# Optimization experiments

Hardware: AMD Instinct MI355X
Metric: run time of the kernel (lower is better)

## Reference

```python
import jax, jax.numpy as jnp
import numpy as np


def _dwconv(x, w, b):
    # depthwise conv, NCHW, kernel [C,1,k,k], SAME padding k//2
    k = w.shape[-1]
    p = k // 2
    out = jax.lax.conv_general_dilated(x, w, (1, 1), [(p, p), (p, p)],
                                       feature_group_count=x.shape[1])
    return out + b[None, :, None, None]


def _conv1x1(x, W, b):
    return jnp.einsum('oc,bchw->bohw', W, x) + b[None, :, None, None]


def _ca_weight(q, k):
    # q,k: [b,c,h,w] -> energy [b,h,w,h+w]
    eH = jnp.einsum('bchw,bcgw->bhwg', q, k)  # attend along H (column)
    eW = jnp.einsum('bchw,bchv->bhwv', q, k)  # attend along W (row)
    return jnp.concatenate([eH, eW], axis=3)


def _ca_map(att, v):
    # att: [b,h,w,h+w], v: [b,c,h,w]
    h = v.shape[2]
    outH = jnp.einsum('bcgw,bhwg->bchw', v, att[..., :h])
    outW = jnp.einsum('bchv,bhwv->bchw', v, att[..., h:])
    return outH + outW


def _cc_block(cnn, Wq, bq, Wk, bk, Wv, bv, gamma):
    q = _conv1x1(cnn, Wq, bq)
    k = _conv1x1(cnn, Wk, bk)
    v = _conv1x1(cnn, Wv, bv)
    att = jax.nn.softmax(_ca_weight(q, k), axis=1)  # softmax over H axis, as in torch F.softmax(energy, 1)
    return gamma * _ca_map(att, v) + cnn


def _ppeg(x, w7, b7, w5, b5, w3, b3, H, W):
    C = x.shape[1]
    cnn = x.T.reshape(1, C, H, W)
    out = _dwconv(cnn, w7, b7) + cnn + _dwconv(cnn, w5, b5) + _dwconv(cnn, w3, b3)
    return out.reshape(C, H * W).T  # [N, C]


def setup_inputs() -> dict:
    key = jax.random.key(0)
    N, DIM, HID, QK = 65536, 1024, 512, 64  # N = 256^2
    ks = jax.random.split(key, 26)
    s = 0.02
    inp = {
        'h0': jax.random.normal(ks[0], (N, DIM), jnp.float32),
        'w7': jax.random.normal(ks[1], (DIM, 1, 7, 7)) * s,
        'b7': jax.random.normal(ks[2], (DIM,)) * s,
        'w5': jax.random.normal(ks[3], (DIM, 1, 5, 5)) * s,
        'b5': jax.random.normal(ks[4], (DIM,)) * s,
        'w3': jax.random.normal(ks[5], (DIM, 1, 3, 3)) * s,
        'b3': jax.random.normal(ks[6], (DIM,)) * s,
        'W1': jax.random.normal(ks[7], (HID, DIM)) * s,
        'b1': jax.random.normal(ks[8], (HID,)) * s,
        'Wq': jax.random.normal(ks[9], (QK, HID)) * s,
        'bq': jax.random.normal(ks[10], (QK,)) * s,
        'Wk': jax.random.normal(ks[11], (QK, HID)) * s,
        'bk': jax.random.normal(ks[12], (QK,)) * s,
        'Wv': jax.random.normal(ks[13], (HID, HID)) * s,
        'bv': jax.random.normal(ks[14], (HID,)) * s,
        'gamma': jax.random.normal(ks[15], ()) * 0.5,
        'Wq1': jax.random.normal(ks[16], (QK, HID)) * s,
        'bq1': jax.random.normal(ks[17], (QK,)) * s,
        'Wk1': jax.random.normal(ks[18], (QK, HID)) * s,
        'bk1': jax.random.normal(ks[19], (QK,)) * s,
        'Wv1': jax.random.normal(ks[20], (HID, HID)) * s,
        'bv1': jax.random.normal(ks[21], (HID,)) * s,
        'gamma1': jax.random.normal(ks[22], ()) * 0.5,
        'Wfc': jax.random.normal(ks[23], (1, HID)) * s,
        'bfc': jax.random.normal(ks[24], (1,)) * s,
    }
    return inp


def reference(h0, w7, b7, w5, b5, w3, b3, W1, b1,
              Wq, bq, Wk, bk, Wv, bv, gamma,
              Wq1, bq1, Wk1, bk1, Wv1, bv1, gamma1, Wfc, bfc):
    N = h0.shape[0]
    side = int(np.ceil(np.sqrt(N)))
    pad = side * side - N
    h1 = jnp.concatenate([h0, h0[:pad]], axis=0) if pad > 0 else h0
    # PPEG positional encoding (multi-kernel depthwise conv)
    h1 = _ppeg(h1, w7, b7, w5, b5, w3, b3, side, side)
    # fc1: Linear(1024->512) + ReLU  (h1 already square -> second pad is no-op)
    h2 = jax.nn.relu(h1 @ W1.T + b1)  # [N, 512]
    # CCAttention (two criss-cross blocks + fc to 1 logit)
    cnn = h2.T.reshape(1, h2.shape[1], side, side)
    out = _cc_block(cnn, Wq, bq, Wk, bk, Wv, bv, gamma)
    out1 = _cc_block(out, Wq1, bq1, Wk1, bk1, Wv1, bv1, gamma1)
    out1 = out1.reshape(out1.shape[1], side * side).T  # [N, 512]
    logits = out1 @ Wfc.T + bfc  # [N, 1]
    A = jax.nn.softmax(logits.T, axis=1)  # [1, N] attention over instances
    return A
```

## Files before the change

### kernel.cpp

```cpp
#include <hip/hip_runtime.h>

#define HW 65536
#define SIDE 256

typedef __attribute__((ext_vector_type(8))) short short8v;
typedef __attribute__((ext_vector_type(4))) float f32x4;
typedef __attribute__((ext_vector_type(8))) ushort ushort8v;

__device__ __forceinline__ ushort f2bf(float f) {
  unsigned int u = __builtin_bit_cast(unsigned int, f);
  u = (u + 0x7fff + ((u >> 16) & 1)) >> 16;
  return (ushort)u;
}
__device__ __forceinline__ float bf2f(unsigned int u) {
  return __builtin_bit_cast(float, (u & 0xffffu) << 16);
}
__device__ __forceinline__ float bflo(unsigned int d) {
  return __builtin_bit_cast(float, d << 16);
}
__device__ __forceinline__ float bfhi(unsigned int d) {
  return __builtin_bit_cast(float, d & 0xffff0000u);
}
__device__ __forceinline__ void gld16(const void* g, void* l) {
  __builtin_amdgcn_global_load_lds(
      (const __attribute__((address_space(1))) void*)g,
      (__attribute__((address_space(3))) void*)l, 16, 0, 0);
}

__global__ __launch_bounds__(256) void k_prep(
    const float* __restrict__ W1, const float* __restrict__ Wv,
    const float* __restrict__ Wv1, const float* __restrict__ Wq,
    const float* __restrict__ Wk, const float* __restrict__ Wq1,
    const float* __restrict__ Wk1, const float* __restrict__ bq,
    const float* __restrict__ bk, const float* __restrict__ bq1,
    const float* __restrict__ bk1, const float* __restrict__ w7,
    const float* __restrict__ b7, const float* __restrict__ w5,
    const float* __restrict__ b5, const float* __restrict__ w3,
    const float* __restrict__ b3,
    ushort* __restrict__ W1b, ushort* __restrict__ Wvb,
    ushort* __restrict__ Wv1b, ushort* __restrict__ Wqkb,
    ushort* __restrict__ Wqk1b, float* __restrict__ bqk,
    float* __restrict__ bqk1, float* __restrict__ wc, float* __restrict__ bc) {
  const int i = blockIdx.x * 256 + threadIdx.x;
  if (i < 524288) { W1b[i] = f2bf(W1[i]); return; }
  if (i < 786432) { int j = i - 524288; Wvb[j] = f2bf(Wv[j]); return; }
  if (i < 1048576) { int j = i - 786432; Wv1b[j] = f2bf(Wv1[j]); return; }
  if (i < 1081344) { int j = i - 1048576; Wqkb[j] = f2bf(Wq[j]); return; }
  if (i < 1114112) { int j = i - 1081344; Wqkb[32768 + j] = f2bf(Wk[j]); return; }
  if (i < 1146880) { int j = i - 1114112; Wqk1b[j] = f2bf(Wq1[j]); return; }
  if (i < 1179648) { int j = i - 1146880; Wqk1b[32768 + j] = f2bf(Wk1[j]); return; }
  if (i < 1179904) {
    int j = i - 1179648;
    if (j < 64) bqk[j] = bq[j];
    else if (j < 128) bqk[j] = bk[j - 64];
    else if (j < 192) bqk1[j - 128] = bq1[j - 128];
    else bqk1[j - 128] = bk1[j - 192];
    return;
  }
  if (i < 1180928) {
    const int c = i - 1179904;
    float w[49];
#pragma unroll
    for (int t = 0; t < 49; t++) w[t] = w7[c * 49 + t];
    for (int dy = 0; dy < 5; dy++)
      for (int dx = 0; dx < 5; dx++)
        w[(dy + 1) * 7 + (dx + 1)] += w5[c * 25 + dy * 5 + dx];
    for (int dy = 0; dy < 3; dy++)
      for (int dx = 0; dx < 3; dx++)
        w[(dy + 2) * 7 + (dx + 2)] += w3[c * 9 + dy * 3 + dx];
    w[3 * 7 + 3] += 1.0f;
#pragma unroll
    for (int t = 0; t < 49; t++) wc[c * 49 + t] = w[t];
    bc[c] = b7[c] + b5[c] + b3[c];
  }
}

__global__ __launch_bounds__(256) void k_transpose_nc_v(
    const float* __restrict__ in, ushort* __restrict__ out) {
  __shared__ ushort t[64][64];
  const int c0 = blockIdx.x << 6, r0 = blockIdx.y << 6;
  const int tid = threadIdx.x;
#pragma unroll
  for (int p = 0; p < 2; p++) {
    const int r = (tid >> 3) + p * 32, c8 = tid & 7;
    const float4 f0 = *(const float4*)&in[(size_t)(r0 + r) * 1024 + c0 + c8 * 8];
    const float4 f1 = *(const float4*)&in[(size_t)(r0 + r) * 1024 + c0 + c8 * 8 + 4];
    ushort8v v;
    v[0] = f2bf(f0.x); v[1] = f2bf(f0.y); v[2] = f2bf(f0.z); v[3] = f2bf(f0.w);
    v[4] = f2bf(f1.x); v[5] = f2bf(f1.y); v[6] = f2bf(f1.z); v[7] = f2bf(f1.w);
    *(ushort8v*)&t[r][(c8 ^ ((r >> 3) & 7)) * 8] = v;
  }
  __syncthreads();
#pragma unroll
  for (int p = 0; p < 2; p++) {
    const int c = (tid >> 3) + p * 32, r8 = tid & 7;
    ushort8v v;
#pragma unroll
    for (int j = 0; j < 8; j++) {
      const int rr = r8 * 8 + j;
      v[j] = t[rr][(((c >> 3) ^ r8) << 3) + (c & 7)];
    }
    *(ushort8v*)&out[(size_t)(c0 + c) * HW + r0 + r8 * 8] = v;
  }
}

__global__ __launch_bounds__(256) void k_trv(const ushort* __restrict__ in,
    ushort* __restrict__ out, int R, int C, long long bs) {
  __shared__ ushort t[64][64];
  const size_t base = (size_t)blockIdx.z * bs;
  const int c0 = blockIdx.x << 6, r0 = blockIdx.y << 6;
  const int tid = threadIdx.x;
#pragma unroll
  for (int p = 0; p < 2; p++) {
    const int r = (tid >> 3) + p * 32, c8 = tid & 7;
    const ushort8v v = *(const ushort8v*)&in[base + (size_t)(r0 + r) * C + c0 + c8 * 8];
    *(ushort8v*)&t[r][(c8 ^ ((r >> 3) & 7)) * 8] = v;
  }
  __syncthreads();
#pragma unroll
  for (int p = 0; p < 2; p++) {
    const int c = (tid >> 3) + p * 32, r8 = tid & 7;
    ushort8v v;
#pragma unroll
    for (int j = 0; j < 8; j++) {
      const int rr = r8 * 8 + j;
      v[j] = t[rr][(((c >> 3) ^ r8) << 3) + (c & 7)];
    }
    *(ushort8v*)&out[base + (size_t)(c0 + c) * R + r0 + r8 * 8] = v;
  }
}

__global__ __launch_bounds__(256) void k_dwconv7(const ushort* __restrict__ X,
    const float* __restrict__ wc, const float* __restrict__ bc,
    ushort* __restrict__ out) {
  __shared__ ushort tile[38][272];
  const int c = blockIdx.y;
  const int y0 = blockIdx.x << 5;
  const int tid = threadIdx.x;
  const ushort* Xc = X + (size_t)c * HW;

  float w[49];
#pragma unroll
  for (int i = 0; i < 49; i++) w[i] = wc[c * 49 + i];
  const float bcv = bc[c];

  if (tid < 76) {
    const int r = tid >> 1;
    ushort8v z = {0, 0, 0, 0, 0, 0, 0, 0};
    *(ushort8v*)&tile[r][(tid & 1) ? 264 : 0] = z;
  }
  for (int i = tid; i < 38 * 32; i += 256) {
    const int r = i >> 5, j8 = i & 31;
    const int y = y0 - 3 + r;
    ushort8v v = {0, 0, 0, 0, 0, 0, 0, 0};
    if (y >= 0 && y < SIDE) v = *(const ushort8v*)&Xc[y * SIDE + j8 * 8];
    *(ushort8v*)&tile[r][8 + j8 * 8] = v;
  }
  __syncthreads();

  const int t0 = tid & 63;
  const int ry = (tid >> 6) << 3;
  float acc[8][4] = {};
#pragma unroll
  for (int r = 0; r < 14; r++) {
    const uint2 ua = *(const uint2*)&tile[ry + r][(t0 << 2) + 4];
    const uint2 ub = *(const uint2*)&tile[ry + r][(t0 << 2) + 8];
    const uint2 uc = *(const uint2*)&tile[ry + r][(t0 << 2) + 12];
    float rv[12];
    rv[0] = bflo(ua.x); rv[1] = bfhi(ua.x); rv[2] = bflo(ua.y); rv[3] = bfhi(ua.y);
    rv[4] = bflo(ub.x); rv[5] = bfhi(ub.x); rv[6] = bflo(ub.y); rv[7] = bfhi(ub.y);
    rv[8] = bflo(uc.x); rv[9] = bfhi(uc.x); rv[10] = bflo(uc.y); rv[11] = bfhi(uc.y);
#pragma unroll
    for (int m = 0; m < 8; m++) {
      const int dy = r - m;
      if (dy < 0 || dy > 6) continue;
#pragma unroll
      for (int dx = 0; dx < 7; dx++) {
        const float ww = w[dy * 7 + dx];
#pragma unroll
        for (int o = 0; o < 4; o++) acc[m][o] += ww * rv[o + 1 + dx];
      }
    }
  }
#pragma unroll
  for (int m = 0; m < 8; m++) {
    ushort4 o4 = {f2bf(acc[m][0] + bcv), f2bf(acc[m][1] + bcv),
                  f2bf(acc[m][2] + bcv), f2bf(acc[m][3] + bcv)};
    *(ushort4*)&out[(size_t)c * HW + (y0 + ry + m) * SIDE + (t0 << 2)] = o4;
  }
}

template <int BN, int BIAS, int RELU, int OUTF, int OUTB, int SWZ, int TRN>
__global__ __launch_bounds__(256) void k_mm(
    const ushort* __restrict__ A, int lda, long long bsA,
    const ushort* __restrict__ B, int ldb, long long bsB,
    const float* __restrict__ bias,
    float* __restrict__ Cf, ushort* __restrict__ Cb, int ldc, long long bsC,
    ushort* __restrict__ Ct, int ldt, int K) {
  static_assert(BN == 64 || BN == 128, "BN");
  static_assert(!TRN || BN == 128, "TRN needs BN=128");
  constexpr int FN = BN / 32;
  __shared__ __align__(16) ushort SMEM[128 * 32 + BN * 32];
  ushort* As = SMEM;
  ushort* Bs = SMEM + 128 * 32;
  const int tid = threadIdx.x;

  int bx, by, bz;
  if constexpr (SWZ == 0) {
    bx = blockIdx.x; by = blockIdx.y; bz = blockIdx.z;
  } else if constexpr (SWZ == 1) {
    const int id = blockIdx.x, l = id >> 3;
    by = (id & 7) * 64 + (l >> 2); bx = l & 3; bz = 0;
  } else if constexpr (SWZ == 2) {
    const int id = blockIdx.x, l = id >> 3;
    bz = (id & 7) * 32 + (l >> 2); bx = l & 1; by = (l >> 1) & 1;
  } else {
    const int id = blockIdx.x, l = id >> 3;
    bz = (id & 7) * 32 + (l >> 3); bx = l & 3; by = (l >> 2) & 1;
  }

  const int bm = bx << 7, bn = by * BN;
  const long long zA = (long long)bz * bsA;
  const long long zB = (long long)bz * bsB;
  const long long zC = (long long)bz * bsC;

  const int sr = tid >> 2, sq = tid & 3;
  const int sw0 = (sr >> 1) & 3;
  const int sw1 = ((sr + 64) >> 1) & 3;
  const ushort* Ap0 = A + zA + (size_t)(bm + sr) * lda + ((sq ^ sw0) << 3);
  const ushort* Ap1 = A + zA + (size_t)(bm + sr + 64) * lda + ((sq ^ sw1) << 3);
  const ushort* Bp0 = B + zB + (size_t)(bn + sr) * ldb + ((sq ^ sw0) << 3);
  const ushort* Bp1 = nullptr;
  if constexpr (BN == 128)
    Bp1 = B + zB + (size_t)(bn + sr + 64) * ldb + ((sq ^ sw1) << 3);
  ushort* wA0 = &As[sr * 32 + sq * 8];
  ushort* wA1 = &As[(sr + 64) * 32 + sq * 8];
  ushort* wB0 = &Bs[sr * 32 + sq * 8];
  ushort* wB1 = nullptr;
  if constexpr (BN == 128) wB1 = &Bs[(sr + 64) * 32 + sq * 8];

  const int lane = tid & 63, wv = tid >> 6;
  const int wm = wv & 1, wn = wv >> 1;
  const int fr = lane & 15, kq = lane >> 4;
  int offA[4], offB[FN];
#pragma unroll
  for (int mi = 0; mi < 4; mi++) {
    const int row = wm * 64 + mi * 16 + fr;
    offA[mi] = row * 32 + ((kq ^ ((row >> 1) & 3)) << 3);
  }
#pragma unroll
  for (int ni = 0; ni < FN; ni++) {
    const int row = wn * (BN / 2) + ni * 16 + fr;
    offB[ni] = row * 32 + ((kq ^ ((row >> 1) & 3)) << 3);
  }

  f32x4 acc[4][FN];
#pragma unroll
  for (int mi = 0; mi < 4; mi++)
#pragma unroll
    for (int ni = 0; ni < FN; ni++) acc[mi][ni] = (f32x4){0.f, 0.f, 0.f, 0.f};

  for (int k0 = 0; k0 < K; k0 += 32) {
    __syncthreads();
    gld16(Ap0 + k0, wA0);
    gld16(Ap1 + k0, wA1);
    gld16(Bp0 + k0, wB0);
    if constexpr (BN == 128) gld16(Bp1 + k0, wB1);
    __syncthreads();
    short8v a[4], b[FN];
#pragma unroll
    for (int mi = 0; mi < 4; mi++) a[mi] = *(const short8v*)&As[offA[mi]];
#pragma unroll
    for (int ni = 0; ni < FN; ni++) b[ni] = *(const short8v*)&Bs[offB[ni]];
#pragma unroll
    for (int mi = 0; mi < 4; mi++)
#pragma unroll
      for (int ni = 0; ni < FN; ni++)
        acc[mi][ni] = __builtin_amdgcn_mfma_f32_16x16x32_bf16(b[ni], a[mi], acc[mi][ni], 0, 0, 0);
  }

  ushort tb[4][FN][4];
#pragma unroll
  for (int mi = 0; mi < 4; mi++) {
    const int row = bm + wm * 64 + mi * 16 + fr;
    const float bs1 = (BIAS == 1) ? bias[row] : 0.f;
#pragma unroll
    for (int ni = 0; ni < FN; ni++) {
      const int col = bn + wn * (BN / 2) + ni * 16 + (kq << 2);
      float4 v;
      v.x = acc[mi][ni][0]; v.y = acc[mi][ni][1];
      v.z = acc[mi][ni][2]; v.w = acc[mi][ni][3];
      if (BIAS == 1) { v.x += bs1; v.y += bs1; v.z += bs1; v.w += bs1; }
      if (BIAS == 2) {
        const float4 bc4 = *(const float4*)&bias[col];
        v.x += bc4.x; v.y += bc4.y; v.z += bc4.z; v.w += bc4.w;
      }
      if (RELU) {
        v.x = fmaxf(v.x, 0.f); v.y = fmaxf(v.y, 0.f);
        v.z = fmaxf(v.z, 0.f); v.w = fmaxf(v.w, 0.f);
      }
      const ushort4 u = {f2bf(v.x), f2bf(v.y), f2bf(v.z), f2bf(v.w)};
      const size_t idx = (size_t)(zC + (size_t)row * ldc + col);
      if (OUTF) *(float4*)&Cf[idx] = v;
      if (OUTB) *(ushort4*)&Cb[idx] = u;
      if (TRN) {
        tb[mi][ni][0] = u.x; tb[mi][ni][1] = u.y;
        tb[mi][ni][2] = u.z; tb[mi][ni][3] = u.w;
      }
    }
  }

  if constexpr (TRN) {
    ushort* St = SMEM;
#pragma unroll
    for (int hh = 0; hh < 2; hh++) {
      __syncthreads();
      if (wn == hh) {
#pragma unroll
        for (int mi = 0; mi < 4; mi++) {
          const int rloc = wm * 64 + mi * 16 + fr;
#pragma unroll
          for (int ni = 0; ni < 4; ni++) {
            const int cl = ni * 16 + (kq << 2);
#pragma unroll
            for (int r = 0; r < 4; r++)
              St[(cl + r) * 128 + rloc] = tb[mi][ni][r];
          }
        }
      }
      __syncthreads();
      const int n_ = tid >> 2;
#pragma unroll
      for (int j = 0; j < 4; j++) {
        const int ck = (tid & 3) * 4 + j;
        const ushort8v vv = *(const ushort8v*)&St[n_ * 128 + ck * 8];
        *(ushort8v*)&Ct[(size_t)(bn + hh * 64 + n_) * ldt + bm + ck * 8] = vv;
      }
    }
  }
}

__global__ __launch_bounds__(256) void k_softmax2(const ushort* __restrict__ EW,
    ushort* __restrict__ AW, const ushort* __restrict__ EH,
    ushort* __restrict__ AH) {
  int b = blockIdx.x;
  const ushort* E; ushort* A; int os, hs;
  if (b < 256) { E = EW; A = AW; os = 256; hs = HW; }
  else { E = EH; A = AH; os = HW; hs = 256; b -= 256; }
  const size_t base = (size_t)b * os + threadIdx.x;
  float m = -3.4e38f, s = 0.f;
  for (int h = 0; h < 256; h++) {
    const float x = bf2f(E[base + (size_t)h * hs]);
    const float nm = fmaxf(m, x);
    s = s * __expf(m - nm) + __expf(x - nm);
    m = nm;
  }
  const float inv = 1.0f / s;
  for (int h = 0; h < 256; h++) {
    const size_t i = base + (size_t)h * hs;
    A[i] = f2bf(__expf(bf2f(E[i]) - m) * inv);
  }
}

__global__ __launch_bounds__(256) void k_merge3(const ushort* __restrict__ O,
    const ushort* __restrict__ TH, const ushort* __restrict__ CN,
    const float* __restrict__ gammap, ushort* __restrict__ outB) {
  __shared__ ushort t[64][64];
  const float g = *gammap;
  const size_t base = (size_t)blockIdx.z * HW;
  const int h0 = blockIdx.y << 6, w0 = blockIdx.x << 6;
  const int tid = threadIdx.x;
#pragma unroll
  for (int p = 0; p < 2; p++) {
    const int r = (tid >> 3) + p * 32, c8 = tid & 7;
    const ushort8v v = *(const ushort8v*)&TH[base + (w0 + r) * SIDE + h0 + c8 * 8];
    *(ushort8v*)&t[r][(c8 ^ ((r >> 3) & 7)) * 8] = v;
  }
  __syncthreads();
#pragma unroll
  for (int p = 0; p < 2; p++) {
    const int h = (tid >> 3) + p * 32, r8 = tid & 7;
    const size_t idx = base + (h0 + h) * SIDE + w0 + r8 * 8;
    const ushort8v o8 = *(const ushort8v*)&O[idx];
    const ushort8v c8v = *(const ushort8v*)&CN[idx];
    ushort8v res;
#pragma unroll
    for (int j = 0; j < 8; j++) {
      const int rr = r8 * 8 + j;
      const float th = bf2f(t[rr][(((h >> 3) ^ r8) << 3) + (h & 7)]);
      res[j] = f2bf(g * (bf2f(o8[j]) + th) + bf2f(c8v[j]));
    }
    *(ushort8v*)&outB[idx] = res;
  }
}

__global__ __launch_bounds__(256) void k_logits(const ushort* __restrict__ X,
    const float* __restrict__ Wfc, const float* __restrict__ bfc,
    float* __restrict__ L) {
  const int n = blockIdx.x * 256 + threadIdx.x;
  float s = 0.f;
  for (int j = 0; j < 512; j++) s += bf2f(X[(size_t)j * HW + n]) * Wfc[j];
  L[n] = s + bfc[0];
}

__global__ __launch_bounds__(256) void k_smax_reduce(const float* __restrict__ L,
                                                     float* __restrict__ red) {
  __shared__ float sm[256];
  const int tid = threadIdx.x;
  float m = -3.4e38f;
  for (int i = tid; i < HW; i += 256) m = fmaxf(m, L[i]);
  sm[tid] = m;
  __syncthreads();
  for (int s = 128; s > 0; s >>= 1) {
    if (tid < s) sm[tid] = fmaxf(sm[tid], sm[tid + s]);
    __syncthreads();
  }
  const float M = sm[0];
  __syncthreads();
  float sum = 0.f;
  for (int i = tid; i < HW; i += 256) sum += expf(L[i] - M);
  sm[tid] = sum;
  __syncthreads();
  for (int s = 128; s > 0; s >>= 1) {
    if (tid < s) sm[tid] += sm[tid + s];
    __syncthreads();
  }
  if (tid == 0) { red[0] = M; red[1] = sm[0]; }
}

__global__ __launch_bounds__(256) void k_smax_write(const float* __restrict__ L,
    const float* __restrict__ red, float* __restrict__ out) {
  const int n = blockIdx.x * 256 + threadIdx.x;
  out[n] = expf(L[n] - red[0]) * (1.0f / red[1]);
}

extern "C" void kernel_launch(void* const* d_in, const int* in_sizes, int n_in,
                              void* d_out, int out_size, void* d_ws, size_t ws_size,
                              hipStream_t stream) {
  const float* h0 = (const float*)d_in[0];
  const float* w7 = (const float*)d_in[1];
  const float* b7 = (const float*)d_in[2];
  const float* w5 = (const float*)d_in[3];
  const float* b5 = (const float*)d_in[4];
  const float* w3 = (const float*)d_in[5];
  const float* b3 = (const float*)d_in[6];
  const float* W1 = (const float*)d_in[7];
  const float* b1 = (const float*)d_in[8];
  const float* Wq = (const float*)d_in[9];
  const float* bq = (const float*)d_in[10];
  const float* Wk = (const float*)d_in[11];
  const float* bk = (const float*)d_in[12];
  const float* Wv = (const float*)d_in[13];
  const float* bv = (const float*)d_in[14];
  const float* gamma = (const float*)d_in[15];
  const float* Wq1 = (const float*)d_in[16];
  const float* bq1 = (const float*)d_in[17];
  const float* Wk1 = (const float*)d_in[18];
  const float* bk1 = (const float*)d_in[19];
  const float* Wv1 = (const float*)d_in[20];
  const float* bv1 = (const float*)d_in[21];
  const float* gamma1 = (const float*)d_in[22];
  const float* Wfc = (const float*)d_in[23];
  const float* bfc = (const float*)d_in[24];

  char* W = (char*)d_ws;
  const size_t MB = 1 << 20;
  ushort* Xb    = (ushort*)(W + 0);
  ushort* H2b   = (ushort*)(W + 0);
  ushort* H2t   = (ushort*)(W + 64 * MB);
  ushort* qkt   = (ushort*)(W + 128 * MB);
  ushort* AttW  = (ushort*)(W + 144 * MB);
  ushort* AttH  = (ushort*)(W + 176 * MB);
  ushort* H1b   = (ushort*)(W + 256 * MB);
  ushort* H1t   = (ushort*)(W + 384 * MB);
  ushort* Vb    = (ushort*)(W + 384 * MB);
  ushort* vTb   = (ushort*)(W + 448 * MB);
  ushort* Ob    = (ushort*)(W + 512 * MB);
  ushort* THbb  = (ushort*)(W + 576 * MB);
  ushort* EbW   = (ushort*)(W + 640 * MB);
  ushort* EbH   = (ushort*)(W + 672 * MB);
  ushort* W1b   = (ushort*)(W + 704 * MB);
  ushort* Wvb   = (ushort*)(W + 705 * MB);
  ushort* Wv1b  = (ushort*)(W + 705 * MB + 512 * 1024);
  ushort* Wqkb  = (ushort*)(W + 706 * MB);
  ushort* Wqk1b = (ushort*)(W + 706 * MB + 128 * 1024);
  float*  wcomb = (float*)(W + 706 * MB + 256 * 1024);
  float*  bcomb = (float*)(W + 706 * MB + 464 * 1024);
  float*  bqk   = (float*)(W + 706 * MB + 472 * 1024);
  float*  bqk1  = (float*)(W + 706 * MB + 474 * 1024);
  float*  L     = (float*)(W + 707 * MB);
  float*  red   = (float*)(W + 707 * MB + 256 * 1024);

  k_prep<<<4613, 256, 0, stream>>>(W1, Wv, Wv1, Wq, Wk, Wq1, Wk1,
                                   bq, bk, bq1, bk1, w7, b7, w5, b5, w3, b3,
                                   W1b, Wvb, Wv1b, Wqkb, Wqk1b, bqk, bqk1,
                                   wcomb, bcomb);

  k_transpose_nc_v<<<dim3(16, 1024), 256, 0, stream>>>(h0, Xb);
  k_dwconv7<<<dim3(8, 1024), 256, 0, stream>>>(Xb, wcomb, bcomb, H1b);
  k_trv<<<dim3(1024, 16, 1), 256, 0, stream>>>(H1b, H1t, 1024, HW, 0);

  k_mm<128, 1, 1, 0, 1, 1, 1><<<2048, 256, 0, stream>>>(
      W1b, 1024, 0, H1t, 1024, 0, b1, nullptr, H2b, HW, 0, H2t, 512, 1024);

  auto cc_block = [&](const ushort* act, ushort* cnn, const ushort* Wqk_,
                      const float* bqk_, const ushort* Wv_, const float* bv_,
                      const float* gam) {
    k_mm<128, 2, 0, 0, 1, 0, 0><<<dim3(512, 1, 1), 256, 0, stream>>>(
        act, 512, 0, Wqk_, 512, 0, bqk_, nullptr, qkt, 128, 0, nullptr, 0, 512);
    k_mm<128, 1, 0, 0, 1, 1, 0><<<2048, 256, 0, stream>>>(
        Wv_, 512, 0, act, 512, 0, bv_, nullptr, Vb, HW, 0, nullptr, 0, 512);
    k_trv<<<dim3(4, 4, 512), 256, 0, stream>>>(Vb, vTb, 256, 256, 65536);
    k_mm<128, 0, 0, 0, 1, 2, 0><<<1024, 256, 0, stream>>>(
        qkt, 128, 32768, qkt + 64, 128, 32768, nullptr, nullptr, EbW, 256,
        65536, nullptr, 0, 64);
    k_mm<128, 0, 0, 0, 1, 2, 0><<<1024, 256, 0, stream>>>(
        qkt, 32768, 128, qkt + 64, 32768, 128, nullptr, nullptr, EbH, 256,
        65536, nullptr, 0, 64);
    k_softmax2<<<512, 256, 0, stream>>>(EbW, AttW, EbH, AttH);
    k_mm<128, 0, 0, 0, 1, 3, 0><<<2048, 256, 0, stream>>>(
        Vb, HW, 256, AttW, 256, 65536, nullptr, nullptr, Ob, HW, 256,
        nullptr, 0, 256);
    k_mm<128, 0, 0, 0, 1, 3, 0><<<2048, 256, 0, stream>>>(
        vTb, HW, 256, AttH, 256, 65536, nullptr, nullptr, THbb, HW, 256,
        nullptr, 0, 256);
    k_merge3<<<dim3(4, 4, 512), 256, 0, stream>>>(Ob, THbb, cnn, gam, cnn);
  };

  cc_block(H2t, H2b, Wqkb, bqk, Wvb, bv, gamma);
  k_trv<<<dim3(1024, 8, 1), 256, 0, stream>>>(H2b, H2t, 512, HW, 0);
  cc_block(H2t, H2b, Wqk1b, bqk1, Wv1b, bv1, gamma1);

  k_logits<<<256, 256, 0, stream>>>(H2b, Wfc, bfc, L);
  k_smax_reduce<<<1, 256, 0, stream>>>(L, red);
  k_smax_write<<<256, 256, 0, stream>>>(L, red, (float*)d_out);
}
```

Baseline: 1.236 ms.

## Add double-buffered 256x128 GEMM kernel for fc1 and value projections

Introduces k_mm8, a 512-thread GEMM with 256x128 output tiles that double-buffers LDS stages so the global-to-LDS loads for step t+2 overlap the MFMA work of step t. It uses raw s_barrier with explicit waitcnt and raises wave priority around the MFMA block. The new kernel replaces the fc1 GEMM, which also writes a transposed copy, and the V-projection GEMM in both criss-cross blocks. The old TRN and SWZ==1 paths are removed from k_mm. This is meant to hide memory latency and cut the number of per-k-step syncthreads. In exchange it uses more LDS per block and has hand-managed synchronisation that is easy to get wrong.

New measurement: 1.220 ms. No clear change (-1.3%).

```diff
diff --git a/kernel.cpp b/kernel.cpp
--- a/kernel.cpp
+++ b/kernel.cpp
@@ -190,15 +190,157 @@
   }
 }
 
-template <int BN, int BIAS, int RELU, int OUTF, int OUTB, int SWZ, int TRN>
+template <int K, int RELU, int TRN>
+__global__ __launch_bounds__(512) void k_mm8(
+    const ushort* __restrict__ A, int lda,
+    const ushort* __restrict__ B, int ldb,
+    const float* __restrict__ bias,
+    ushort* __restrict__ Cb, int ldc,
+    ushort* __restrict__ Ct, int ldt) {
+  constexpr int NT = K / 32;
+  __shared__ __align__(16) ushort SM[2 * 12288];
+  const int tid = threadIdx.x;
+  const int lane = tid & 63, wv = tid >> 6;
+
+  const int id = blockIdx.x;
+  const int wg = (id & 7) * 128 + (id >> 3);
+  const int bm = (wg >> 9) << 8;
+  const int bn = (wg & 511) << 7;
+
+  const int l4 = lane >> 2;
+  const int sch = (lane & 3) ^ (l4 & 3);
+  const int rA0 = (wv * 2) * 16 + l4;
+  const int rA1 = (wv * 2 + 1) * 16 + l4;
+  const int rB = wv * 16 + l4;
+  const ushort* ApS0 = A + (size_t)(bm + rA0) * lda + sch * 8;
+  const ushort* ApS1 = A + (size_t)(bm + rA1) * lda + sch * 8;
+  const ushort* BpS = B + (size_t)(bn + rB) * ldb + sch * 8;
+  const int dA0 = (wv * 2) * 512 + lane * 8;
+  const int dA1 = (wv * 2 + 1) * 512 + lane * 8;
+  const int dB = wv * 512 + lane * 8;
+
+  const int wm = wv & 3, wn = wv >> 2;
+  const int fr = lane & 15, kq = lane >> 4;
+  int offA[4], offB[4];
+#pragma unroll
+  for (int mi = 0; mi < 4; mi++) {
+    const int row = wm * 64 + mi * 16 + fr;
+    offA[mi] = row * 32 + ((kq ^ (row & 3)) << 3);
+  }
+#pragma unroll
+  for (int ni = 0; ni < 4; ni++) {
+    const int row = wn * 64 + ni * 16 + fr;
+    offB[ni] = 8192 + row * 32 + ((kq ^ (row & 3)) << 3);
+  }
+
+  f32x4 acc[4][4];
+#pragma unroll
+  for (int mi = 0; mi < 4; mi++)
+#pragma unroll
+    for (int ni = 0; ni < 4; ni++) acc[mi][ni] = (f32x4){0.f, 0.f, 0.f, 0.f};
+
+#define STAGE8(bufbase, k0)                         \
+  do {                                              \
+    gld16(ApS0 + (k0), &SM[(bufbase) + dA0]);       \
+    gld16(ApS1 + (k0), &SM[(bufbase) + dA1]);       \
+    gld16(BpS + (k0), &SM[(bufbase) + 8192 + dB]);  \
+  } while (0)
+
+  STAGE8(0, 0);
+  STAGE8(12288, 32);
+  asm volatile("s_waitcnt vmcnt(3)" ::: "memory");
+  __builtin_amdgcn_s_barrier();
+
+  int cur = 0;
+#pragma unroll 2
+  for (int t = 0; t < NT; ++t) {
+    const int base = cur ? 12288 : 0;
+    short8v a[4], b2[4];
+#pragma unroll
+    for (int mi = 0; mi < 4; mi++) a[mi] = *(const short8v*)&SM[base + offA[mi]];
+#pragma unroll
+    for (int ni = 0; ni < 4; ni++) b2[ni] = *(const short8v*)&SM[base + offB[ni]];
+    asm volatile("s_waitcnt lgkmcnt(0)" ::: "memory");
+    __builtin_amdgcn_s_barrier();
+    const int ts = (t + 2 < NT) ? (t + 2) : (NT - 1);
+    STAGE8(base, ts << 5);
+    __builtin_amdgcn_s_setprio(1);
+#pragma unroll
+    for (int mi = 0; mi < 4; mi++)
+#pragma unroll
+      for (int ni = 0; ni < 4; ni++)
+        acc[mi][ni] = __builtin_amdgcn_mfma_f32_16x16x32_bf16(b2[ni], a[mi], acc[mi][ni], 0, 0, 0);
+    __builtin_amdgcn_s_setprio(0);
+    asm volatile("s_waitcnt vmcnt(3)" ::: "memory");
+    __builtin_amdgcn_s_barrier();
+    cur ^= 1;
+  }
+#undef STAGE8
+  asm volatile("s_waitcnt vmcnt(0)" ::: "memory");
+  __builtin_amdgcn_s_barrier();
+
+  ushort tb[4][4][4];
+#pragma unroll
+  for (int mi = 0; mi < 4; mi++) {
+    const int row = bm + wm * 64 + mi * 16 + fr;
+    const float bs1 = bias[row];
+#pragma unroll
+    for (int ni = 0; ni < 4; ni++) {
+      const int col = bn + wn * 64 + ni * 16 + (kq << 2);
+      float4 v;
+      v.x = acc[mi][ni][0] + bs1; v.y = acc[mi][ni][1] + bs1;
+      v.z = acc[mi][ni][2] + bs1; v.w = acc[mi][ni][3] + bs1;
+      if (RELU) {
+        v.x = fmaxf(v.x, 0.f); v.y = fmaxf(v.y, 0.f);
+        v.z = fmaxf(v.z, 0.f); v.w = fmaxf(v.w, 0.f);
+      }
+      const ushort4 u = {f2bf(v.x), f2bf(v.y), f2bf(v.z), f2bf(v.w)};
+      *(ushort4*)&Cb[(size_t)row * ldc + col] = u;
+      if (TRN) {
+        tb[mi][ni][0] = u.x; tb[mi][ni][1] = u.y;
+        tb[mi][ni][2] = u.z; tb[mi][ni][3] = u.w;
+      }
+    }
+  }
+
+  if constexpr (TRN) {
+    ushort* St = SM;
+#pragma unroll
+    for (int hh = 0; hh < 2; hh++) {
+      __builtin_amdgcn_s_barrier();
+      if (wn == hh) {
+#pragma unroll
+        for (int mi = 0; mi < 4; mi++) {
+          const int cl = wm * 64 + mi * 16 + fr;
+#pragma unroll
+          for (int ni = 0; ni < 4; ni++) {
+            const int nl = ni * 16 + (kq << 2);
+#pragma unroll
+            for (int r = 0; r < 4; r++) St[(nl + r) * 256 + cl] = tb[mi][ni][r];
+          }
+        }
+      }
+      __builtin_amdgcn_s_barrier();
+      const int cid = tid * 4;
+      const int rowo = cid >> 5;
+#pragma unroll
+      for (int j = 0; j < 4; j++) {
+        const int ch = (cid + j) & 31;
+        const ushort8v vv = *(const ushort8v*)&St[rowo * 256 + ch * 8];
+        *(ushort8v*)&Ct[(size_t)(bn + hh * 64 + rowo) * ldt + bm + ch * 8] = vv;
+      }
+    }
+  }
+}
+
+template <int BN, int BIAS, int RELU, int OUTF, int OUTB, int SWZ>
 __global__ __launch_bounds__(256) void k_mm(
     const ushort* __restrict__ A, int lda, long long bsA,
     const ushort* __restrict__ B, int ldb, long long bsB,
     const float* __restrict__ bias,
     float* __restrict__ Cf, ushort* __restrict__ Cb, int ldc, long long bsC,
-    ushort* __restrict__ Ct, int ldt, int K) {
+    int K) {
   static_assert(BN == 64 || BN == 128, "BN");
-  static_assert(!TRN || BN == 128, "TRN needs BN=128");
   constexpr int FN = BN / 32;
   __shared__ __align__(16) ushort SMEM[128 * 32 + BN * 32];
   ushort* As = SMEM;
@@ -208,9 +350,6 @@
   int bx, by, bz;
   if constexpr (SWZ == 0) {
     bx = blockIdx.x; by = blockIdx.y; bz = blockIdx.z;
-  } else if constexpr (SWZ == 1) {
-    const int id = blockIdx.x, l = id >> 3;
-    by = (id & 7) * 64 + (l >> 2); bx = l & 3; bz = 0;
   } else if constexpr (SWZ == 2) {
     const int id = blockIdx.x, l = id >> 3;
     bz = (id & 7) * 32 + (l >> 2); bx = l & 1; by = (l >> 1) & 1;
@@ -279,7 +418,6 @@
         acc[mi][ni] = __builtin_amdgcn_mfma_f32_16x16x32_bf16(b[ni], a[mi], acc[mi][ni], 0, 0, 0);
   }
 
-  ushort tb[4][FN][4];
 #pragma unroll
   for (int mi = 0; mi < 4; mi++) {
     const int row = bm + wm * 64 + mi * 16 + fr;
@@ -299,42 +437,11 @@
         v.x = fmaxf(v.x, 0.f); v.y = fmaxf(v.y, 0.f);
         v.z = fmaxf(v.z, 0.f); v.w = fmaxf(v.w, 0.f);
       }
-      const ushort4 u = {f2bf(v.x), f2bf(v.y), f2bf(v.z), f2bf(v.w)};
       const size_t idx = (size_t)(zC + (size_t)row * ldc + col);
       if (OUTF) *(float4*)&Cf[idx] = v;
-      if (OUTB) *(ushort4*)&Cb[idx] = u;
-      if (TRN) {
-        tb[mi][ni][0] = u.x; tb[mi][ni][1] = u.y;
-        tb[mi][ni][2] = u.z; tb[mi][ni][3] = u.w;
-      }
-    }
-  }
-
-  if constexpr (TRN) {
-    ushort* St = SMEM;
-#pragma unroll
-    for (int hh = 0; hh < 2; hh++) {
-      __syncthreads();
-      if (wn == hh) {
-#pragma unroll
-        for (int mi = 0; mi < 4; mi++) {
-          const int rloc = wm * 64 + mi * 16 + fr;
-#pragma unroll
-          for (int ni = 0; ni < 4; ni++) {
-            const int cl = ni * 16 + (kq << 2);
-#pragma unroll
-            for (int r = 0; r < 4; r++)
-              St[(cl + r) * 128 + rloc] = tb[mi][ni][r];
-          }
-        }
-      }
-      __syncthreads();
-      const int n_ = tid >> 2;
-#pragma unroll
-      for (int j = 0; j < 4; j++) {
-        const int ck = (tid & 3) * 4 + j;
-        const ushort8v vv = *(const ushort8v*)&St[n_ * 128 + ck * 8];
-        *(ushort8v*)&Ct[(size_t)(bn + hh * 64 + n_) * ldt + bm + ck * 8] = vv;
+      if (OUTB) {
+        ushort4 u = {f2bf(v.x), f2bf(v.y), f2bf(v.z), f2bf(v.w)};
+        *(ushort4*)&Cb[idx] = u;
       }
     }
   }
@@ -500,30 +607,28 @@
   k_dwconv7<<<dim3(8, 1024), 256, 0, stream>>>(Xb, wcomb, bcomb, H1b);
   k_trv<<<dim3(1024, 16, 1), 256, 0, stream>>>(H1b, H1t, 1024, HW, 0);
 
-  k_mm<128, 1, 1, 0, 1, 1, 1><<<2048, 256, 0, stream>>>(
-      W1b, 1024, 0, H1t, 1024, 0, b1, nullptr, H2b, HW, 0, H2t, 512, 1024);
+  k_mm8<1024, 1, 1><<<1024, 512, 0, stream>>>(
+      W1b, 1024, H1t, 1024, b1, H2b, HW, H2t, 512);
 
   auto cc_block = [&](const ushort* act, ushort* cnn, const ushort* Wqk_,
                       const float* bqk_, const ushort* Wv_, const float* bv_,
                       const float* gam) {
-    k_mm<128, 2, 0, 0, 1, 0, 0><<<dim3(512, 1, 1), 256, 0, stream>>>(
-        act, 512, 0, Wqk_, 512, 0, bqk_, nullptr, qkt, 128, 0, nullptr, 0, 512);
-    k_mm<128, 1, 0, 0, 1, 1, 0><<<2048, 256, 0, stream>>>(
-        Wv_, 512, 0, act, 512, 0, bv_, nullptr, Vb, HW, 0, nullptr, 0, 512);
+    k_mm<128, 2, 0, 0, 1, 0><<<dim3(512, 1, 1), 256, 0, stream>>>(
+        act, 512, 0, Wqk_, 512, 0, bqk_, nullptr, qkt, 128, 0, 512);
+    k_mm8<512, 0, 0><<<1024, 512, 0, stream>>>(
+        Wv_, 512, act, 512, bv_, Vb, HW, nullptr, 0);
     k_trv<<<dim3(4, 4, 512), 256, 0, stream>>>(Vb, vTb, 256, 256, 65536);
-    k_mm<128, 0, 0, 0, 1, 2, 0><<<1024, 256, 0, stream>>>(
+    k_mm<128, 0, 0, 0, 1, 2><<<1024, 256, 0, stream>>>(
         qkt, 128, 32768, qkt + 64, 128, 32768, nullptr, nullptr, EbW, 256,
-        65536, nullptr, 0, 64);
-    k_mm<128, 0, 0, 0, 1, 2, 0><<<1024, 256, 0, stream>>>(
+        65536, 64);
+    k_mm<128, 0, 0, 0, 1, 2><<<1024, 256, 0, stream>>>(
         qkt, 32768, 128, qkt + 64, 32768, 128, nullptr, nullptr, EbH, 256,
-        65536, nullptr, 0, 64);
+        65536, 64);
     k_softmax2<<<512, 256, 0, stream>>>(EbW, AttW, EbH, AttH);
-    k_mm<128, 0, 0, 0, 1, 3, 0><<<2048, 256, 0, stream>>>(
-        Vb, HW, 256, AttW, 256, 65536, nullptr, nullptr, Ob, HW, 256,
-        nullptr, 0, 256);
-    k_mm<128, 0, 0, 0, 1, 3, 0><<<2048, 256, 0, stream>>>(
-        vTb, HW, 256, AttH, 256, 65536, nullptr, nullptr, THbb, HW, 256,
-        nullptr, 0, 256);
+    k_mm<128, 0, 0, 0, 1, 3><<<2048, 256, 0, stream>>>(
+        Vb, HW, 256, AttW, 256, 65536, nullptr, nullptr, Ob, HW, 256, 256);
+    k_mm<128, 0, 0, 0, 1, 3><<<2048, 256, 0, stream>>>(
+        vTb, HW, 256, AttH, 256, 65536, nullptr, nullptr, THbb, HW, 256, 256);
     k_merge3<<<dim3(4, 4, 512), 256, 0, stream>>>(Ob, THbb, cnn, gam, cnn);
   };
 
```
